# Performance work log

Hardware: AMD Instinct MI355X
Metric: run time of the kernel (lower is better)

Reference implementation:

```python
import jax, jax.numpy as jnp
import numpy as np

N_NODES = 50000
N_EDGES = 800000
IN_F = 128
H_F = 128
OUT_F = 128
N_GRAPHS = 128


def setup_inputs() -> dict:
    key = jax.random.key(0)
    ks = jax.random.split(key, 7)
    x = jax.random.normal(ks[0], (N_NODES, IN_F), dtype=jnp.float32)
    edge_index = jax.random.randint(ks[1], (2, N_EDGES), 0, N_NODES, dtype=jnp.int32)
    batch = jnp.sort(jax.random.randint(ks[2], (N_NODES,), 0, N_GRAPHS, dtype=jnp.int32))
    s1 = 1.0 / np.sqrt(IN_F)
    s2 = 1.0 / np.sqrt(H_F)
    W1 = jax.random.uniform(ks[3], (IN_F, H_F), jnp.float32, -s1, s1)
    b1 = jnp.zeros((H_F,), jnp.float32)
    W2 = jax.random.uniform(ks[4], (H_F, OUT_F), jnp.float32, -s2, s2)
    b2 = jnp.zeros((OUT_F,), jnp.float32)
    return {"x": x, "edge_index": edge_index, "batch": batch,
            "W1": W1, "b1": b1, "W2": W2, "b2": b2}


def _gcn_conv(x, W, b, src, dst, n_nodes):
    # PyG GCNConv: out = D^{-1/2} (A + I) D^{-1/2} (x W) + b
    h = x @ W  # [N, out]
    # degree including self-loop
    deg = jax.ops.segment_sum(jnp.ones_like(dst, dtype=h.dtype), dst,
                              num_segments=n_nodes) + 1.0
    dinv = jax.lax.rsqrt(deg)  # [N]
    norm = dinv[src] * dinv[dst]  # [E]
    agg = jax.ops.segment_sum(h[src] * norm[:, None], dst, num_segments=n_nodes)
    # self-loop term has norm dinv[i]^2
    return agg + (dinv * dinv)[:, None] * h + b


def reference(x, edge_index, batch, W1, b1, W2, b2):
    src, dst = edge_index[0], edge_index[1]
    h = jax.nn.relu(_gcn_conv(x, W1, b1, src, dst, N_NODES))
    h = _gcn_conv(h, W2, b2, src, dst, N_NODES)
    # global_add_pool over graphs
    return jax.ops.segment_sum(h, batch, num_segments=N_GRAPHS)
```

## Files before the change

kernel.cpp:

```cpp
#include <hip/hip_runtime.h>
#include <hip/hip_bf16.h>


typedef _Float16 f16x8 __attribute__((ext_vector_type(8)));
typedef float f32x4 __attribute__((ext_vector_type(4)));

#define BCHUNK 4096

__global__ __launch_bounds__(256) void bin_hist(const int* __restrict__ ei,
                                                const float* __restrict__ W1,
                                                _Float16* __restrict__ wfrag,
                                                float* __restrict__ P,
                                                _Float16* __restrict__ hb,
                                                _Float16* __restrict__ ob,
                                                int* __restrict__ counts,
                                                int E, int N, int NB, int NBLK) {
    __shared__ int hist[256];
    int t = threadIdx.x, blk = blockIdx.x;
    int gtid = blk * 256 + t;
    int gstride = gridDim.x * 256;

    for (int i = gtid; i < 128 * 128; i += gstride) P[i] = 0.f;
    if (gtid < 64) {
        ((unsigned int*)(hb + (size_t)N * 128))[gtid] = 0u;
        ((unsigned int*)(ob + (size_t)N * 128))[gtid] = 0u;
    }
    if (gtid < 2048) {
        int lane = gtid & 63, kc = (gtid >> 6) & 3, nb = gtid >> 8;
        int col = nb * 16 + (lane & 15);
        int krow = kc * 32 + (lane >> 4) * 8;
#pragma unroll
        for (int j = 0; j < 8; j++)
            wfrag[gtid * 8 + j] = (_Float16)W1[(krow + j) * 128 + col];
    }

    for (int b = t; b < NB; b += 256) hist[b] = 0;
    __syncthreads();
    int base = blk * BCHUNK;
    int end = min(E, base + BCHUNK);
    for (int e = base + t; e < end; e += 256)
        atomicAdd(&hist[ei[E + e] >> 8], 1);
    __syncthreads();
    for (int b = t; b < NB; b += 256) counts[b * NBLK + blk] = hist[b];
}


__global__ void block_sums(const int* __restrict__ data, int* __restrict__ bsum, int n) {
    __shared__ int s[256];
    int base = blockIdx.x * 1024;
    int t = threadIdx.x;
    int v = 0;
#pragma unroll
    for (int i = 0; i < 4; i++) {
        int idx = base + t * 4 + i;
        if (idx < n) v += data[idx];
    }
    s[t] = v;
    __syncthreads();
    for (int off = 128; off > 0; off >>= 1) {
        if (t < off) s[t] += s[t + off];
        __syncthreads();
    }
    if (t == 0) bsum[blockIdx.x] = s[0];
}

__global__ void block_sums_pad(const int* __restrict__ data, int* __restrict__ bsum, int n) {
    __shared__ int s[256];
    int base = blockIdx.x * 1024;
    int t = threadIdx.x;
    int v = 0;
#pragma unroll
    for (int i = 0; i < 4; i++) {
        int idx = base + t * 4 + i;
        if (idx < n) v += (data[idx] + 7) & ~7;
    }
    s[t] = v;
    __syncthreads();
    for (int off = 128; off > 0; off >>= 1) {
        if (t < off) s[t] += s[t + off];
        __syncthreads();
    }
    if (t == 0) bsum[blockIdx.x] = s[0];
}

__global__ void scan_bsum(int* __restrict__ bsum, int nb) {
    int lane = threadIdx.x & 63;
    int v = (lane < nb) ? bsum[lane] : 0;
    int incl = v;
#pragma unroll
    for (int off = 1; off < 64; off *= 2) {
        int u = __shfl_up(incl, off);
        if (lane >= off) incl += u;
    }
    if (lane < nb) bsum[lane] = incl - v;
}

__global__ void scan_apply(int* __restrict__ data, const int* __restrict__ bsum, int n) {
    __shared__ int s[256];
    int base = blockIdx.x * 1024;
    int t = threadIdx.x;
    int loc[4];
    int v = 0;
#pragma unroll
    for (int i = 0; i < 4; i++) {
        int idx = base + t * 4 + i;
        loc[i] = (idx < n) ? data[idx] : 0;
        v += loc[i];
    }
    s[t] = v;
    __syncthreads();
    for (int off = 1; off < 256; off *= 2) {
        int u = (t >= off) ? s[t - off] : 0;
        __syncthreads();
        s[t] += u;
        __syncthreads();
    }
    int excl = s[t] - v + bsum[blockIdx.x];
#pragma unroll
    for (int i = 0; i < 4; i++) {
        int idx = base + t * 4 + i;
        if (idx < n) { data[idx] = excl; excl += loc[i]; }
    }
}

__global__ void scan_nodes(const int* __restrict__ cnt, const int* __restrict__ bsum,
                           int* __restrict__ row_start, float* __restrict__ dinv, int n) {
    __shared__ int s[256];
    int base = blockIdx.x * 1024;
    int t = threadIdx.x;
    int loc[4], pc[4];
    int v = 0;
#pragma unroll
    for (int i = 0; i < 4; i++) {
        int idx = base + t * 4 + i;
        loc[i] = (idx < n) ? cnt[idx] : 0;
        pc[i] = (loc[i] + 7) & ~7;
        v += pc[i];
    }
    s[t] = v;
    __syncthreads();
    for (int off = 1; off < 256; off *= 2) {
        int u = (t >= off) ? s[t - off] : 0;
        __syncthreads();
        s[t] += u;
        __syncthreads();
    }
    int excl = s[t] - v + bsum[blockIdx.x];
#pragma unroll
    for (int i = 0; i < 4; i++) {
        int idx = base + t * 4 + i;
        if (idx < n) {
            row_start[idx] = excl;
            dinv[idx] = rsqrtf((float)loc[i] + 1.0f);
            excl += pc[i];
        }
    }
}


__global__ __launch_bounds__(256) void bin_scatter(const int* __restrict__ ei,
                                                   const int* __restrict__ counts,
                                                   unsigned int* __restrict__ bedges,
                                                   int E, int NB, int NBLK) {
    __shared__ int lcur[256];
    int t = threadIdx.x, blk = blockIdx.x;
    for (int b = t; b < NB; b += 256) lcur[b] = counts[b * NBLK + blk];
    __syncthreads();
    int base = blk * BCHUNK;
    int end = min(E, base + BCHUNK);
    for (int e = base + t; e < end; e += 256) {
        int s = ei[e];
        int d = ei[E + e];
        int pos = atomicAdd(&lcur[d >> 8], 1);
        bedges[pos] = (unsigned int)s | ((unsigned int)(d & 255) << 16);
    }
}

__global__ __launch_bounds__(256) void deg_buckets(const unsigned int* __restrict__ bedges,
                                                   const int* __restrict__ counts,
                                                   int* __restrict__ cnt,
                                                   int E, int N, int NB, int NBLK) {
    __shared__ int lcnt[256];
    int b = blockIdx.x, t = threadIdx.x;
    lcnt[t] = 0;
    __syncthreads();
    int bstart = counts[b * NBLK];
    int bend = (b + 1 < NB) ? counts[(b + 1) * NBLK] : E;
    for (int i = bstart + t; i < bend; i += 256)
        atomicAdd(&lcnt[bedges[i] >> 16], 1);
    __syncthreads();
    int node = (b << 8) + t;
    if (node < N) cnt[node] = lcnt[t];
}

__global__ __launch_bounds__(256) void fill_buckets(const unsigned int* __restrict__ bedges,
                                                    const int* __restrict__ counts,
                                                    const int* __restrict__ row_start,
                                                    const int* __restrict__ cnt,
                                                    int* __restrict__ srcs,
                                                    int E, int N, int NB, int NBLK) {
    __shared__ int lcur[256];
    int b = blockIdx.x, t = threadIdx.x;
    int node = (b << 8) + t;
    lcur[t] = (node < N) ? row_start[node] : 0;
    __syncthreads();
    int bstart = counts[b * NBLK];
    int bend = (b + 1 < NB) ? counts[(b + 1) * NBLK] : E;
    for (int i = bstart + t; i < bend; i += 256) {
        unsigned int p = bedges[i];
        int pos = atomicAdd(&lcur[p >> 16], 1);
        srcs[pos] = (int)(p & 0xffffu);
    }
    if (node < N) {
        int c = cnt[node];
        int e0 = row_start[node] + c;
        int e1 = row_start[node] + ((c + 7) & ~7);
        for (int j = e0; j < e1; j++) srcs[j] = N;
    }
}

__global__ __launch_bounds__(256) void gemm_mfma_f32in(const float* __restrict__ A,
                                                       const _Float16* __restrict__ wfrag,
                                                       const float* __restrict__ dinv,
                                                       _Float16* __restrict__ C, int M) {
    __shared__ _Float16 As[128 * 136];
    int t = threadIdx.x;
    int row0 = blockIdx.x * 128;

    const float4* A4 = (const float4*)A;
#pragma unroll
    for (int it = 0; it < 16; it++) {
        int v = it * 256 + t;
        int row = v >> 5;
        int seg = v & 31;
        float4 val = make_float4(0.f, 0.f, 0.f, 0.f);
        if (row0 + row < M) val = A4[(size_t)(row0 + row) * 32 + seg];
        _Float16* pp = &As[row * 136 + seg * 4];
        pp[0] = (_Float16)val.x; pp[1] = (_Float16)val.y;
        pp[2] = (_Float16)val.z; pp[3] = (_Float16)val.w;
    }
    __syncthreads();

    int wv = t >> 6;
    int lane = t & 63;
    int lrow = lane & 15;
    int lq = lane >> 4;

    f32x4 acc[2][8];
#pragma unroll
    for (int i = 0; i < 2; i++)
#pragma unroll
        for (int j = 0; j < 8; j++) acc[i][j] = (f32x4){0.f, 0.f, 0.f, 0.f};

#pragma unroll
    for (int kc = 0; kc < 4; kc++) {
        int k0 = kc * 32;
        f16x8 a0 = *((const f16x8*)&As[(wv * 32 + lrow) * 136 + k0 + lq * 8]);
        f16x8 a1 = *((const f16x8*)&As[(wv * 32 + 16 + lrow) * 136 + k0 + lq * 8]);
#pragma unroll
        for (int nb = 0; nb < 8; nb++) {
            f16x8 b = ((const f16x8*)wfrag)[(nb * 4 + kc) * 64 + lane];
            acc[0][nb] = __builtin_amdgcn_mfma_f32_16x16x32_f16(a0, b, acc[0][nb], 0, 0, 0);
            acc[1][nb] = __builtin_amdgcn_mfma_f32_16x16x32_f16(a1, b, acc[1][nb], 0, 0, 0);
        }
    }

#pragma unroll
    for (int ti = 0; ti < 2; ti++) {
#pragma unroll
        for (int r = 0; r < 4; r++) {
            int row = row0 + wv * 32 + ti * 16 + lq * 4 + r;
            if (row < M) {
                float dv = dinv[row];
#pragma unroll
                for (int nb = 0; nb < 8; nb++)
                    C[(size_t)row * 128 + nb * 16 + lrow] = (_Float16)(acc[ti][nb][r] * dv);
            }
        }
    }
}

__global__ __launch_bounds__(256) void agg1(const _Float16* __restrict__ hb,
                                            const int* __restrict__ srcs,
                                            const int* __restrict__ row_start,
                                            const int* __restrict__ cnt,
                                            const float* __restrict__ dinv,
                                            const float* __restrict__ bias,
                                            _Float16* __restrict__ ob, int n) {
    int node = blockIdx.x * 4 + (threadIdx.x >> 6);
    if (node >= n) return;
    int lane = threadIdx.x & 63;
    int cc = lane & 15;
    int sg = lane >> 4;
    int s0 = row_start[node];
    int c = cnt[node];
    int nit = (c + 7) >> 3;
    float dn = dinv[node];

    float acc[8];
#pragma unroll
    for (int j = 0; j < 8; j++) acc[j] = 0.f;

    const int* sp = srcs + s0;
    int i0 = 0, i1 = 0;
    if (nit > 0) { i0 = sp[sg]; i1 = sp[4 + sg]; }
    for (int it = 0; it < nit; it++) {
        int cs0 = i0, cs1 = i1;
        int nxt = (it + 1 < nit) ? (it + 1) : it;
        i0 = sp[nxt * 8 + sg]; i1 = sp[nxt * 8 + 4 + sg];
        f16x8 v0 = *((const f16x8*)&hb[(size_t)(unsigned)cs0 * 128 + cc * 8]);
        f16x8 v1 = *((const f16x8*)&hb[(size_t)(unsigned)cs1 * 128 + cc * 8]);
#pragma unroll
        for (int j = 0; j < 8; j++) acc[j] += (float)v0[j];
#pragma unroll
        for (int j = 0; j < 8; j++) acc[j] += (float)v1[j];
    }
#pragma unroll
    for (int j = 0; j < 8; j++) {
        acc[j] += __shfl_xor(acc[j], 16);
        acc[j] += __shfl_xor(acc[j], 32);
    }
    f16x8 hs = *((const f16x8*)&hb[(size_t)node * 128 + cc * 8]);
    float4 b0 = ((const float4*)bias)[cc * 2];
    float4 b1v = ((const float4*)bias)[cc * 2 + 1];
    float bb[8] = {b0.x, b0.y, b0.z, b0.w, b1v.x, b1v.y, b1v.z, b1v.w};
    f16x8 o;
#pragma unroll
    for (int j = 0; j < 8; j++) {
        float tv = acc[j] + (float)hs[j];
        tv = fmaxf(fmaf(dn, tv, bb[j]), 0.f) * dn;
        o[j] = (_Float16)tv;
    }
    if (sg == 0) *((f16x8*)&ob[(size_t)node * 128 + cc * 8]) = o;
}

__global__ __launch_bounds__(256) void agg2_pool(const _Float16* __restrict__ ob,
                                                 const int* __restrict__ srcs,
                                                 const int* __restrict__ row_start,
                                                 const int* __restrict__ cnt,
                                                 const float* __restrict__ dinv,
                                                 const int* __restrict__ batch,
                                                 float* __restrict__ P, int n) {
    __shared__ float red[4][128];
    int wv = threadIdx.x >> 6;
    int lane = threadIdx.x & 63;
    int cc = lane & 15;
    int sg = lane >> 4;
    int base = blockIdx.x * 4;
    int node = base + wv;

    float t8[8];
#pragma unroll
    for (int j = 0; j < 8; j++) t8[j] = 0.f;
    int g = -1;

    if (node < n) {
        g = batch[node];
        int s0 = row_start[node];
        int c = cnt[node];
        int nit = (c + 7) >> 3;
        float dn = dinv[node];

        float acc[8];
#pragma unroll
        for (int j = 0; j < 8; j++) acc[j] = 0.f;
        const int* sp = srcs + s0;
        int i0 = 0, i1 = 0;
        if (nit > 0) { i0 = sp[sg]; i1 = sp[4 + sg]; }
        for (int it = 0; it < nit; it++) {
            int cs0 = i0, cs1 = i1;
            int nxt = (it + 1 < nit) ? (it + 1) : it;
            i0 = sp[nxt * 8 + sg]; i1 = sp[nxt * 8 + 4 + sg];
            f16x8 v0 = *((const f16x8*)&ob[(size_t)(unsigned)cs0 * 128 + cc * 8]);
            f16x8 v1 = *((const f16x8*)&ob[(size_t)(unsigned)cs1 * 128 + cc * 8]);
#pragma unroll
            for (int j = 0; j < 8; j++) acc[j] += (float)v0[j];
#pragma unroll
            for (int j = 0; j < 8; j++) acc[j] += (float)v1[j];
        }
#pragma unroll
        for (int j = 0; j < 8; j++) {
            acc[j] += __shfl_xor(acc[j], 16);
            acc[j] += __shfl_xor(acc[j], 32);
        }
        f16x8 hs = *((const f16x8*)&ob[(size_t)node * 128 + cc * 8]);
#pragma unroll
        for (int j = 0; j < 8; j++) t8[j] = dn * (acc[j] + (float)hs[j]);
    }

    int lastn = min(base + 3, n - 1);
    bool uniform = (base < n) && (batch[base] == batch[lastn]) && (base + 3 < n);
    if (uniform) {
        if (sg == 0) {
#pragma unroll
            for (int j = 0; j < 8; j++) red[wv][cc * 8 + j] = t8[j];
        }
        __syncthreads();
        if (wv == 0) {
            int col = lane * 2;
            float sx = red[0][col] + red[1][col] + red[2][col] + red[3][col];
            float sy = red[0][col + 1] + red[1][col + 1] + red[2][col + 1] + red[3][col + 1];
            atomicAdd(&P[g * 128 + col], sx);
            atomicAdd(&P[g * 128 + col + 1], sy);
        }
    } else if (node < n) {
        if (sg == 0) {
#pragma unroll
            for (int j = 0; j < 8; j++) atomicAdd(&P[g * 128 + cc * 8 + j], t8[j]);
        }
    }
}

__global__ __launch_bounds__(128) void gemm_small(const float* __restrict__ P,
                                                  const float* __restrict__ W2,
                                                  const float* __restrict__ b2,
                                                  const int* __restrict__ batch,
                                                  float* __restrict__ out, int n) {
    __shared__ float prow[128];
    int g = blockIdx.x;
    int c = threadIdx.x;
    prow[c] = P[g * 128 + c];
    __syncthreads();
    int lo = 0, hi = n;
    while (lo < hi) { int mid = (lo + hi) >> 1; if (batch[mid] < g) lo = mid + 1; else hi = mid; }
    int start = lo;
    hi = n;
    while (lo < hi) { int mid = (lo + hi) >> 1; if (batch[mid] < g + 1) lo = mid + 1; else hi = mid; }
    float ng = (float)(lo - start);
    float acc = 0.f;
#pragma unroll 8
    for (int k = 0; k < 128; k++) acc = fmaf(prow[k], W2[k * 128 + c], acc);
    out[g * 128 + c] = acc + ng * b2[c];
}

extern "C" void kernel_launch(void* const* d_in, const int* in_sizes, int n_in,
                              void* d_out, int out_size, void* d_ws, size_t ws_size,
                              hipStream_t stream) {
    const float* x  = (const float*)d_in[0];
    const int*   ei = (const int*)d_in[1];
    const int*   batch = (const int*)d_in[2];
    const float* W1 = (const float*)d_in[3];
    const float* b1 = (const float*)d_in[4];
    const float* W2 = (const float*)d_in[5];
    const float* b2 = (const float*)d_in[6];
    float* out = (float*)d_out;

    const int N = in_sizes[2];
    const int E = in_sizes[1] / 2;
    const int G = out_size / 128;

    const int NB = (N + 255) >> 8;
    const int NBLK = (E + BCHUNK - 1) / BCHUNK;
    const int ncounts = NB * NBLK;
    const int SRP = E + 7 * N + 16;

    _Float16* hb = (_Float16*)d_ws;
    _Float16* ob = hb + (size_t)(N + 8) * 128;
    int* cnt  = (int*)(ob + (size_t)(N + 8) * 128);
    int* row_start = cnt + N;
    float* dinv    = (float*)(row_start + N);
    int* srcs      = (int*)(dinv + N);
    unsigned int* bedges = (unsigned int*)(srcs + SRP);
    int* counts    = (int*)(bedges + E);
    _Float16* wfrag1 = (_Float16*)(counts + ncounts);
    float* P       = (float*)(wfrag1 + 128 * 128);
    int* bsum      = (int*)(P + 128 * 128);

    const int nbc = (ncounts + 1023) / 1024;
    const int nbn = (N + 1023) / 1024;

    bin_hist<<<NBLK, 256, 0, stream>>>(ei, W1, wfrag1, P, hb, ob, counts, E, N, NB, NBLK);
    block_sums<<<nbc, 256, 0, stream>>>(counts, bsum, ncounts);
    scan_bsum<<<1, 64, 0, stream>>>(bsum, nbc);
    scan_apply<<<nbc, 256, 0, stream>>>(counts, bsum, ncounts);
    bin_scatter<<<NBLK, 256, 0, stream>>>(ei, counts, bedges, E, NB, NBLK);
    deg_buckets<<<NB, 256, 0, stream>>>(bedges, counts, cnt, E, N, NB, NBLK);
    block_sums_pad<<<nbn, 256, 0, stream>>>(cnt, bsum, N);
    scan_bsum<<<1, 64, 0, stream>>>(bsum, nbn);
    scan_nodes<<<nbn, 256, 0, stream>>>(cnt, bsum, row_start, dinv, N);
    fill_buckets<<<NB, 256, 0, stream>>>(bedges, counts, row_start, cnt, srcs, E, N, NB, NBLK);

    gemm_mfma_f32in<<<(N + 127) / 128, 256, 0, stream>>>(x, wfrag1, dinv, hb, N);
    agg1<<<(N + 3) / 4, 256, 0, stream>>>(hb, srcs, row_start, cnt, dinv, b1, ob, N);
    agg2_pool<<<(N + 3) / 4, 256, 0, stream>>>(ob, srcs, row_start, cnt, dinv, batch, P, N);
    gemm_small<<<G, 128, 0, stream>>>(P, W2, b2, batch, out, N);
}
```

Before: 223.3 us.

## Replace global scans with fixed-capacity bucket segments and fused CSR build

Replaces the multi-kernel global prefix scans over bucket counts and node degrees with a per-bucket segmented scan using fixed-capacity bucket regions, and fuses degree counting, row-start scan, dinv, and source fill into one build_csr kernel. This removes several small kernel launches and one pass over the binned edges. It risks overflow if any 256-node bucket receives more than the fixed capacity of edges, and it enlarges workspace layout.

After: 217.6 us. 1.03x faster.

```diff
diff --git a/kernel.cpp b/kernel.cpp
--- a/kernel.cpp
+++ b/kernel.cpp
@@ -44,119 +44,30 @@
     for (int b = t; b < NB; b += 256) counts[b * NBLK + blk] = hist[b];
 }
 
-
-__global__ void block_sums(const int* __restrict__ data, int* __restrict__ bsum, int n) {
+__global__ __launch_bounds__(256) void scan_counts_seg(int* __restrict__ counts,
+                                                       int* __restrict__ btot,
+                                                       int NBLK, int BCAP) {
     __shared__ int s[256];
-    int base = blockIdx.x * 1024;
-    int t = threadIdx.x;
-    int v = 0;
-#pragma unroll
-    for (int i = 0; i < 4; i++) {
-        int idx = base + t * 4 + i;
-        if (idx < n) v += data[idx];
-    }
-    s[t] = v;
-    __syncthreads();
-    for (int off = 128; off > 0; off >>= 1) {
-        if (t < off) s[t] += s[t + off];
-        __syncthreads();
-    }
-    if (t == 0) bsum[blockIdx.x] = s[0];
-}
-
-__global__ void block_sums_pad(const int* __restrict__ data, int* __restrict__ bsum, int n) {
-    __shared__ int s[256];
-    int base = blockIdx.x * 1024;
-    int t = threadIdx.x;
-    int v = 0;
-#pragma unroll
-    for (int i = 0; i < 4; i++) {
-        int idx = base + t * 4 + i;
-        if (idx < n) v += (data[idx] + 7) & ~7;
-    }
-    s[t] = v;
-    __syncthreads();
-    for (int off = 128; off > 0; off >>= 1) {
-        if (t < off) s[t] += s[t + off];
-        __syncthreads();
-    }
-    if (t == 0) bsum[blockIdx.x] = s[0];
-}
-
-__global__ void scan_bsum(int* __restrict__ bsum, int nb) {
-    int lane = threadIdx.x & 63;
-    int v = (lane < nb) ? bsum[lane] : 0;
-    int incl = v;
-#pragma unroll
-    for (int off = 1; off < 64; off *= 2) {
-        int u = __shfl_up(incl, off);
-        if (lane >= off) incl += u;
-    }
-    if (lane < nb) bsum[lane] = incl - v;
-}
-
-__global__ void scan_apply(int* __restrict__ data, const int* __restrict__ bsum, int n) {
-    __shared__ int s[256];
-    int base = blockIdx.x * 1024;
-    int t = threadIdx.x;
-    int loc[4];
-    int v = 0;
-#pragma unroll
-    for (int i = 0; i < 4; i++) {
-        int idx = base + t * 4 + i;
-        loc[i] = (idx < n) ? data[idx] : 0;
-        v += loc[i];
-    }
-    s[t] = v;
-    __syncthreads();
-    for (int off = 1; off < 256; off *= 2) {
-        int u = (t >= off) ? s[t - off] : 0;
-        __syncthreads();
-        s[t] += u;
-        __syncthreads();
-    }
-    int excl = s[t] - v + bsum[blockIdx.x];
-#pragma unroll
-    for (int i = 0; i < 4; i++) {
-        int idx = base + t * 4 + i;
-        if (idx < n) { data[idx] = excl; excl += loc[i]; }
-    }
-}
-
-__global__ void scan_nodes(const int* __restrict__ cnt, const int* __restrict__ bsum,
-                           int* __restrict__ row_start, float* __restrict__ dinv, int n) {
-    __shared__ int s[256];
-    int base = blockIdx.x * 1024;
-    int t = threadIdx.x;
-    int loc[4], pc[4];
-    int v = 0;
-#pragma unroll
-    for (int i = 0; i < 4; i++) {
-        int idx = base + t * 4 + i;
-        loc[i] = (idx < n) ? cnt[idx] : 0;
-        pc[i] = (loc[i] + 7) & ~7;
-        v += pc[i];
-    }
-    s[t] = v;
-    __syncthreads();
-    for (int off = 1; off < 256; off *= 2) {
-        int u = (t >= off) ? s[t - off] : 0;
-        __syncthreads();
-        s[t] += u;
-        __syncthreads();
-    }
-    int excl = s[t] - v + bsum[blockIdx.x];
-#pragma unroll
-    for (int i = 0; i < 4; i++) {
-        int idx = base + t * 4 + i;
-        if (idx < n) {
-            row_start[idx] = excl;
-            dinv[idx] = rsqrtf((float)loc[i] + 1.0f);
-            excl += pc[i];
-        }
-    }
-}
-
+    int b = blockIdx.x, t = threadIdx.x;
+    int carry = 0;
+    for (int base = 0; base < NBLK; base += 256) {
+        int idx = base + t;
+        int v = (idx < NBLK) ? counts[b * NBLK + idx] : 0;
+        s[t] = v;
+        __syncthreads();
+        for (int off = 1; off < 256; off *= 2) {
+            int u = (t >= off) ? s[t - off] : 0;
+            __syncthreads();
+            s[t] += u;
+            __syncthreads();
+        }
+        int excl = s[t] - v + carry;
+        if (idx < NBLK) counts[b * NBLK + idx] = b * BCAP + excl;
+        carry += s[255];
+        __syncthreads();
+    }
+    if (t == 0) btot[b] = carry;
+}
 
 __global__ __launch_bounds__(256) void bin_scatter(const int* __restrict__ ei,
                                                    const int* __restrict__ counts,
@@ -176,46 +87,50 @@
     }
 }
 
-__global__ __launch_bounds__(256) void deg_buckets(const unsigned int* __restrict__ bedges,
-                                                   const int* __restrict__ counts,
-                                                   int* __restrict__ cnt,
-                                                   int E, int N, int NB, int NBLK) {
+__global__ __launch_bounds__(256) void build_csr(const unsigned int* __restrict__ bedges,
+                                                 const int* __restrict__ btot,
+                                                 int* __restrict__ cnt,
+                                                 int* __restrict__ row_start,
+                                                 float* __restrict__ dinv,
+                                                 int* __restrict__ srcs,
+                                                 int N, int BCAP, int SCAP) {
     __shared__ int lcnt[256];
-    int b = blockIdx.x, t = threadIdx.x;
-    lcnt[t] = 0;
-    __syncthreads();
-    int bstart = counts[b * NBLK];
-    int bend = (b + 1 < NB) ? counts[(b + 1) * NBLK] : E;
-    for (int i = bstart + t; i < bend; i += 256)
-        atomicAdd(&lcnt[bedges[i] >> 16], 1);
-    __syncthreads();
-    int node = (b << 8) + t;
-    if (node < N) cnt[node] = lcnt[t];
-}
-
-__global__ __launch_bounds__(256) void fill_buckets(const unsigned int* __restrict__ bedges,
-                                                    const int* __restrict__ counts,
-                                                    const int* __restrict__ row_start,
-                                                    const int* __restrict__ cnt,
-                                                    int* __restrict__ srcs,
-                                                    int E, int N, int NB, int NBLK) {
+    __shared__ int lpre[256];
     __shared__ int lcur[256];
     int b = blockIdx.x, t = threadIdx.x;
     int node = (b << 8) + t;
-    lcur[t] = (node < N) ? row_start[node] : 0;
-    __syncthreads();
-    int bstart = counts[b * NBLK];
-    int bend = (b + 1 < NB) ? counts[(b + 1) * NBLK] : E;
+    lcnt[t] = 0;
+    __syncthreads();
+    int bstart = b * BCAP;
+    int bend = bstart + btot[b];
+    for (int i = bstart + t; i < bend; i += 256)
+        atomicAdd(&lcnt[bedges[i] >> 16], 1);
+    __syncthreads();
+    int c = lcnt[t];
+    int pc = (c + 7) & ~7;
+    lpre[t] = pc;
+    __syncthreads();
+    for (int off = 1; off < 256; off *= 2) {
+        int u = (t >= off) ? lpre[t - off] : 0;
+        __syncthreads();
+        lpre[t] += u;
+        __syncthreads();
+    }
+    int rs = b * SCAP + lpre[t] - pc;
+    if (node < N) {
+        row_start[node] = rs;
+        cnt[node] = c;
+        dinv[node] = rsqrtf((float)c + 1.0f);
+    }
+    lcur[t] = rs;
+    __syncthreads();
     for (int i = bstart + t; i < bend; i += 256) {
         unsigned int p = bedges[i];
         int pos = atomicAdd(&lcur[p >> 16], 1);
         srcs[pos] = (int)(p & 0xffffu);
     }
     if (node < N) {
-        int c = cnt[node];
-        int e0 = row_start[node] + c;
-        int e1 = row_start[node] + ((c + 7) & ~7);
-        for (int j = e0; j < e1; j++) srcs[j] = N;
+        for (int j = rs + c; j < rs + pc; j++) srcs[j] = N;
     }
 }
 
@@ -452,7 +367,8 @@
     const int NB = (N + 255) >> 8;
     const int NBLK = (E + BCHUNK - 1) / BCHUNK;
     const int ncounts = NB * NBLK;
-    const int SRP = E + 7 * N + 16;
+    const int BCAP = 8192;
+    const int SCAP = BCAP + 2048;
 
     _Float16* hb = (_Float16*)d_ws;
     _Float16* ob = hb + (size_t)(N + 8) * 128;
@@ -460,25 +376,16 @@
     int* row_start = cnt + N;
     float* dinv    = (float*)(row_start + N);
     int* srcs      = (int*)(dinv + N);
-    unsigned int* bedges = (unsigned int*)(srcs + SRP);
-    int* counts    = (int*)(bedges + E);
-    _Float16* wfrag1 = (_Float16*)(counts + ncounts);
+    unsigned int* bedges = (unsigned int*)(srcs + (size_t)NB * SCAP);
+    int* counts    = (int*)(bedges + (size_t)NB * BCAP);
+    int* btot      = counts + ncounts;
+    _Float16* wfrag1 = (_Float16*)(btot + NB);
     float* P       = (float*)(wfrag1 + 128 * 128);
-    int* bsum      = (int*)(P + 128 * 128);
-
-    const int nbc = (ncounts + 1023) / 1024;
-    const int nbn = (N + 1023) / 1024;
 
     bin_hist<<<NBLK, 256, 0, stream>>>(ei, W1, wfrag1, P, hb, ob, counts, E, N, NB, NBLK);
-    block_sums<<<nbc, 256, 0, stream>>>(counts, bsum, ncounts);
-    scan_bsum<<<1, 64, 0, stream>>>(bsum, nbc);
-    scan_apply<<<nbc, 256, 0, stream>>>(counts, bsum, ncounts);
+    scan_counts_seg<<<NB, 256, 0, stream>>>(counts, btot, NBLK, BCAP);
     bin_scatter<<<NBLK, 256, 0, stream>>>(ei, counts, bedges, E, NB, NBLK);
-    deg_buckets<<<NB, 256, 0, stream>>>(bedges, counts, cnt, E, N, NB, NBLK);
-    block_sums_pad<<<nbn, 256, 0, stream>>>(cnt, bsum, N);
-    scan_bsum<<<1, 64, 0, stream>>>(bsum, nbn);
-    scan_nodes<<<nbn, 256, 0, stream>>>(cnt, bsum, row_start, dinv, N);
-    fill_buckets<<<NB, 256, 0, stream>>>(bedges, counts, row_start, cnt, srcs, E, N, NB, NBLK);
+    build_csr<<<NB, 256, 0, stream>>>(bedges, btot, cnt, row_start, dinv, srcs, N, BCAP, SCAP);
 
     gemm_mfma_f32in<<<(N + 127) / 128, 256, 0, stream>>>(x, wfrag1, dinv, hb, N);
     agg1<<<(N + 3) / 4, 256, 0, stream>>>(hb, srcs, row_start, cnt, dinv, b1, ob, N);
```
